# Kernel tuning notes

Measured on AMD Instinct MI355X. Metric: run time of the kernel, lower is better.

The kernel has to match this reference:

```python
import jax, jax.numpy as jnp
import numpy as np

NUM_HEADS = 32
KV_HEADS = 8
HEAD_DIM = 64
HIDDEN = 2048
ROPE_THETA = 10000.0


def setup_inputs() -> dict:
    key = jax.random.key(0)
    ks = jax.random.split(key, 5)
    B, S, H = 2, 2048, HIDDEN
    scale = 0.02
    return {
        "x": jax.random.normal(ks[0], (B, S, H), dtype=jnp.float32),
        # weights stored as (in_features, out_features)
        "Wq": jax.random.normal(ks[1], (H, NUM_HEADS * HEAD_DIM), dtype=jnp.float32) * scale,
        "Wk": jax.random.normal(ks[2], (H, KV_HEADS * HEAD_DIM), dtype=jnp.float32) * scale,
        "Wv": jax.random.normal(ks[3], (H, KV_HEADS * HEAD_DIM), dtype=jnp.float32) * scale,
        "Wo": jax.random.normal(ks[4], (H, H), dtype=jnp.float32) * scale,
    }


def _rope_tables(seq_len, dtype):
    # freq over even dims, angles concatenated twice -> (S, HEAD_DIM)
    freq = 1.0 / (ROPE_THETA ** (jnp.arange(0, HEAD_DIM, 2, dtype=jnp.float32) / HEAD_DIM))
    ang = jnp.arange(seq_len, dtype=jnp.float32)[:, None] * freq[None, :]
    emb = jnp.concatenate([ang, ang], axis=-1)
    return jnp.cos(emb).astype(dtype), jnp.sin(emb).astype(dtype)


def _rotate_half(x):
    x1, x2 = jnp.split(x, 2, axis=-1)
    return jnp.concatenate([-x2, x1], axis=-1)


def reference(x, Wq, Wk, Wv, Wo):
    B, S, H = x.shape
    q = jnp.einsum("bsd,df->bsf", x, Wq).reshape(B, S, NUM_HEADS, HEAD_DIM).transpose(0, 2, 1, 3)
    k = jnp.einsum("bsd,df->bsf", x, Wk).reshape(B, S, KV_HEADS, HEAD_DIM).transpose(0, 2, 1, 3)
    v = jnp.einsum("bsd,df->bsf", x, Wv).reshape(B, S, KV_HEADS, HEAD_DIM).transpose(0, 2, 1, 3)

    cos, sin = _rope_tables(S, x.dtype)  # (S, HEAD_DIM), broadcasts over (B, h, S, D)
    q = q * cos + _rotate_half(q) * sin
    k = k * cos + _rotate_half(k) * sin

    n_rep = NUM_HEADS // KV_HEADS
    k = jnp.repeat(k, n_rep, axis=1)  # (B, NUM_HEADS, S, D)
    v = jnp.repeat(v, n_rep, axis=1)

    scores = jnp.einsum("bhsd,bhtd->bhst", q, k) / jnp.sqrt(jnp.asarray(HEAD_DIM, x.dtype))
    weights = jax.nn.softmax(scores, axis=-1)
    ctx = jnp.einsum("bhst,bhtd->bhsd", weights, v)
    ctx = ctx.transpose(0, 2, 1, 3).reshape(B, S, H)
    return jnp.einsum("bsd,df->bsf", ctx, Wo)
```

## Files before the change

### kernel.cpp

```cpp
#include <hip/hip_runtime.h>

typedef short s8v __attribute__((ext_vector_type(8)));
typedef short s4v __attribute__((ext_vector_type(4)));
typedef unsigned u4v __attribute__((ext_vector_type(4)));
typedef int i2v __attribute__((ext_vector_type(2)));
typedef float f2v __attribute__((ext_vector_type(2)));
typedef float f4v __attribute__((ext_vector_type(4)));

typedef const __attribute__((address_space(1))) char* gp1_t;
typedef __attribute__((address_space(3))) char* lp3_t;

__device__ __forceinline__ float bf2f(short s) {
    union { unsigned u; float f; } c;
    c.u = ((unsigned)(unsigned short)s) << 16;
    return c.f;
}
__device__ __forceinline__ short f2bf(float f) {
    union { float f; unsigned u; } c; c.f = f;
    unsigned r = (c.u + 0x7FFFu + ((c.u >> 16) & 1u)) >> 16;
    return (short)r;
}
__device__ __forceinline__ unsigned cvt_pk_bf16(float a, float b) {
    unsigned r;
    asm("v_cvt_pk_bf16_f32 %0, %1, %2" : "=v"(r) : "v"(a), "v"(b));
    return r;
}
__device__ __forceinline__ s8v cvt8(const float* __restrict__ p) {
    f4v a = *(const f4v*)p;
    f4v b = *(const f4v*)(p + 4);
    s8v r;
    r[0] = f2bf(a[0]); r[1] = f2bf(a[1]); r[2] = f2bf(a[2]); r[3] = f2bf(a[3]);
    r[4] = f2bf(b[0]); r[5] = f2bf(b[1]); r[6] = f2bf(b[2]); r[7] = f2bf(b[3]);
    return r;
}


__global__ __launch_bounds__(256) void cvt_x(const float* __restrict__ x,
                                             short* __restrict__ xb) {
    long i = ((long)blockIdx.x * 256 + threadIdx.x) * 8;
    *(s8v*)&xb[i] = cvt8(&x[i]);
}

__global__ __launch_bounds__(256) void cvt_wt(const float* __restrict__ W,
                                              short* __restrict__ Wt,
                                              int N, int obase, float scale) {
    __shared__ __align__(16) short tile[64 * 72];
    const int kt = blockIdx.y * 64, n0 = blockIdx.x * 64;
    const int t = threadIdx.x;
    const int r = t >> 4, c4 = (t & 15) * 4;
#pragma unroll
    for (int i = 0; i < 4; i++) {
        int kr = r + i * 16;
        f4v v = *(const f4v*)&W[(long)(kt + kr) * N + n0 + c4];
#pragma unroll
        for (int j = 0; j < 4; j++) tile[(c4 + j) * 72 + kr] = f2bf(v[j] * scale);
    }
    __syncthreads();
    const int nr = t >> 3, kc = (t & 7) * 8;
#pragma unroll
    for (int i = 0; i < 2; i++) {
        int n = nr + i * 32;
        *(s8v*)&Wt[(long)(obase + n0 + n) * 2048 + kt + kc] = *(const s8v*)&tile[n * 72 + kc];
    }
}

template <bool CF32, bool ROPE>
__global__ __launch_bounds__(512, 2) void gemm_bt8(const short* __restrict__ A,
                                                   const short* __restrict__ Bt,
                                                   void* __restrict__ Cv,
                                                   int K, int lda, int ldb, int ldc) {
    __shared__ __align__(16) short Ab[2][16384];
    __shared__ __align__(16) short Bb[2][16384];

    const int tid = threadIdx.x;
    const int lane = tid & 63;
    const int wave = tid >> 6;
    const int quad = lane >> 4;
    const int l15 = lane & 15;

    const int nwg = gridDim.x * gridDim.y;
    int f = blockIdx.y * gridDim.x + blockIdx.x;
    if ((nwg & 7) == 0) f = (f & 7) * (nwg >> 3) + (f >> 3);
    const int m0 = (f / gridDim.x) * 256;
    const int n0 = (f % gridDim.x) * 256;

    const int wm = (wave >> 2) * 128;
    const int wn = (wave & 3) * 64;

    const int rsub = lane >> 3;
    const int sslot = (lane & 7) ^ rsub;
    const short* aS[2][2];
    const short* bS[2][2];
#pragma unroll
    for (int h = 0; h < 2; h++)
#pragma unroll
        for (int i = 0; i < 2; i++) {
            int row = h * 128 + wave * 16 + i * 8 + rsub;
            aS[h][i] = A  + (long)(m0 + row) * lda + sslot * 8;
            bS[h][i] = Bt + (long)(n0 + row) * ldb + sslot * 8;
        }

    auto stageA = [&](int buf, int h, int kt) {
        char* d = (char*)&Ab[buf][0] + h * 16384 + wave * 2048;
        __builtin_amdgcn_global_load_lds((gp1_t)(aS[h][0] + (long)kt * 64), (lp3_t)d, 16, 0, 0);
        __builtin_amdgcn_global_load_lds((gp1_t)(aS[h][1] + (long)kt * 64), (lp3_t)(d + 1024), 16, 0, 0);
    };
    auto stageB = [&](int buf, int h, int kt) {
        char* d = (char*)&Bb[buf][0] + h * 16384 + wave * 2048;
        __builtin_amdgcn_global_load_lds((gp1_t)(bS[h][0] + (long)kt * 64), (lp3_t)d, 16, 0, 0);
        __builtin_amdgcn_global_load_lds((gp1_t)(bS[h][1] + (long)kt * 64), (lp3_t)(d + 1024), 16, 0, 0);
    };

    const int ks0 = (quad ^ (l15 & 7)) * 8;
    const int ks1 = ks0 ^ 32;

    f4v acc[2][4][2][2];
#pragma unroll
    for (int a = 0; a < 2; a++)
#pragma unroll
        for (int b = 0; b < 4; b++)
#pragma unroll
            for (int c = 0; c < 2; c++)
#pragma unroll
                for (int d = 0; d < 2; d++) acc[a][b][c][d] = (f4v){0.f, 0.f, 0.f, 0.f};

    const int NT = K >> 6;

    stageB(0, 0, 0); stageB(0, 1, 0); stageA(0, 0, 0); stageA(0, 1, 0);
    stageB(1, 0, 1); stageB(1, 1, 1); stageA(1, 0, 1);
    asm volatile("s_waitcnt vmcnt(6)" ::: "memory");
    __builtin_amdgcn_s_barrier();

    for (int t = 0; t < NT; ++t) {
        const short* Ac = &Ab[t & 1][0];
        const short* Bc = &Bb[t & 1][0];
        const int nb = (t + 1) & 1;
        s8v af[4][2], bf0[2][2], bf1[2][2];

#pragma unroll
        for (int mi = 0; mi < 4; mi++) {
            const int row = wm + mi * 16 + l15;
            af[mi][0] = *(const s8v*)&Ac[row * 64 + ks0];
            af[mi][1] = *(const s8v*)&Ac[row * 64 + ks1];
        }
#pragma unroll
        for (int ni = 0; ni < 2; ni++) {
            const int row = wn + ni * 16 + l15;
            bf0[ni][0] = *(const s8v*)&Bc[row * 64 + ks0];
            bf0[ni][1] = *(const s8v*)&Bc[row * 64 + ks1];
        }
        if (t + 1 < NT) stageA(nb, 1, t + 1);
        __builtin_amdgcn_s_setprio(1);
#pragma unroll
        for (int mi = 0; mi < 4; mi++)
#pragma unroll
            for (int ni = 0; ni < 2; ni++) {
                acc[0][mi][0][ni] = __builtin_amdgcn_mfma_f32_16x16x32_bf16(af[mi][0], bf0[ni][0], acc[0][mi][0][ni], 0, 0, 0);
                acc[0][mi][0][ni] = __builtin_amdgcn_mfma_f32_16x16x32_bf16(af[mi][1], bf0[ni][1], acc[0][mi][0][ni], 0, 0, 0);
            }
        __builtin_amdgcn_s_setprio(0);
        __builtin_amdgcn_s_barrier();

#pragma unroll
        for (int ni = 0; ni < 2; ni++) {
            const int row = wn + 32 + ni * 16 + l15;
            bf1[ni][0] = *(const s8v*)&Bc[row * 64 + ks0];
            bf1[ni][1] = *(const s8v*)&Bc[row * 64 + ks1];
        }
        __builtin_amdgcn_s_setprio(1);
#pragma unroll
        for (int mi = 0; mi < 4; mi++)
#pragma unroll
            for (int ni = 0; ni < 2; ni++) {
                acc[0][mi][1][ni] = __builtin_amdgcn_mfma_f32_16x16x32_bf16(af[mi][0], bf1[ni][0], acc[0][mi][1][ni], 0, 0, 0);
                acc[0][mi][1][ni] = __builtin_amdgcn_mfma_f32_16x16x32_bf16(af[mi][1], bf1[ni][1], acc[0][mi][1][ni], 0, 0, 0);
            }
        __builtin_amdgcn_s_setprio(0);
        __builtin_amdgcn_s_barrier();

#pragma unroll
        for (int mi = 0; mi < 4; mi++) {
            const int row = wm + 64 + mi * 16 + l15;
            af[mi][0] = *(const s8v*)&Ac[row * 64 + ks0];
            af[mi][1] = *(const s8v*)&Ac[row * 64 + ks1];
        }
        if (t + 2 < NT) stageB(t & 1, 0, t + 2);
        __builtin_amdgcn_s_setprio(1);
#pragma unroll
        for (int mi = 0; mi < 4; mi++)
#pragma unroll
            for (int ni = 0; ni < 2; ni++) {
                acc[1][mi][0][ni] = __builtin_amdgcn_mfma_f32_16x16x32_bf16(af[mi][0], bf0[ni][0], acc[1][mi][0][ni], 0, 0, 0);
                acc[1][mi][0][ni] = __builtin_amdgcn_mfma_f32_16x16x32_bf16(af[mi][1], bf0[ni][1], acc[1][mi][0][ni], 0, 0, 0);
            }
        __builtin_amdgcn_s_setprio(0);
        __builtin_amdgcn_s_barrier();

        if (t + 2 < NT) { stageB(t & 1, 1, t + 2); stageA(t & 1, 0, t + 2); }
        __builtin_amdgcn_s_setprio(1);
#pragma unroll
        for (int mi = 0; mi < 4; mi++)
#pragma unroll
            for (int ni = 0; ni < 2; ni++) {
                acc[1][mi][1][ni] = __builtin_amdgcn_mfma_f32_16x16x32_bf16(af[mi][0], bf1[ni][0], acc[1][mi][1][ni], 0, 0, 0);
                acc[1][mi][1][ni] = __builtin_amdgcn_mfma_f32_16x16x32_bf16(af[mi][1], bf1[ni][1], acc[1][mi][1][ni], 0, 0, 0);
            }
        __builtin_amdgcn_s_setprio(0);
        if (t + 1 < NT) {
            if (t + 1 == NT - 1) asm volatile("s_waitcnt vmcnt(0)" ::: "memory");
            else                 asm volatile("s_waitcnt vmcnt(6)" ::: "memory");
            __builtin_amdgcn_s_barrier();
        }
    }

    if (ROPE && (n0 + wn) < 2560) {
        const float NLOG = -0.4152410118609203f;
        const float fr0 = exp2f((float)l15 * NLOG);
        const float fr1 = exp2f((float)(16 + l15) * NLOG);
#pragma unroll
        for (int qm = 0; qm < 2; qm++)
#pragma unroll
            for (int mi = 0; mi < 4; mi++)
#pragma unroll
                for (int r = 0; r < 4; r++) {
                    const float s = (float)((m0 + wm + qm * 64 + mi * 16 + quad * 4 + r) & 2047);
#pragma unroll
                    for (int ni = 0; ni < 2; ni++) {
                        float sn, cs;
                        __sincosf(s * (ni ? fr1 : fr0), &sn, &cs);
                        float x1 = acc[qm][mi][0][ni][r];
                        float x2 = acc[qm][mi][1][ni][r];
                        acc[qm][mi][0][ni][r] = x1 * cs - x2 * sn;
                        acc[qm][mi][1][ni][r] = x2 * cs + x1 * sn;
                    }
                }
    }

#pragma unroll
    for (int qm = 0; qm < 2; qm++)
#pragma unroll
        for (int mi = 0; mi < 4; mi++)
#pragma unroll
            for (int qn = 0; qn < 2; qn++)
#pragma unroll
                for (int ni = 0; ni < 2; ni++)
#pragma unroll
                    for (int r = 0; r < 4; r++) {
                        int row = m0 + wm + qm * 64 + mi * 16 + quad * 4 + r;
                        int col = n0 + wn + qn * 32 + ni * 16 + l15;
                        float v = acc[qm][mi][qn][ni][r];
                        if (CF32) ((float*)Cv)[(long)row * ldc + col] = v;
                        else      ((short*)Cv)[(long)row * ldc + col] = f2bf(v);
                    }
}

template <bool CF32>
__global__ __launch_bounds__(512, 2) void gemm_bt2(const short* __restrict__ A,
                                                   const short* __restrict__ Bt,
                                                   void* __restrict__ Cv,
                                                   int K, int lda, int ldb, int ldc) {
    __shared__ __align__(16) short Ab[2][8192];
    __shared__ __align__(16) short Bb[2][16384];

    const int tid = threadIdx.x;
    const int lane = tid & 63;
    const int wave = tid >> 6;
    const int quad = lane >> 4;
    const int l15 = lane & 15;

    const int nwg = gridDim.x * gridDim.y;
    int f = blockIdx.y * gridDim.x + blockIdx.x;
    if ((nwg & 7) == 0) f = (f & 7) * (nwg >> 3) + (f >> 3);
    const int m0 = (f / gridDim.x) * 128;
    const int n0 = (f % gridDim.x) * 256;

    const int wm = (wave >> 2) * 64;
    const int wn = (wave & 3) * 64;

    const int rsub = lane >> 3;
    const int sslot = (lane & 7) ^ rsub;
    const short* aS[2];
    const short* bS[4];
#pragma unroll
    for (int i = 0; i < 2; i++)
        aS[i] = A + (long)(m0 + wave * 16 + i * 8 + rsub) * lda + sslot * 8;
#pragma unroll
    for (int i = 0; i < 4; i++)
        bS[i] = Bt + (long)(n0 + wave * 32 + i * 8 + rsub) * ldb + sslot * 8;

    auto stageA = [&](int buf, int kt) {
        char* d = (char*)&Ab[buf][0] + wave * 2048;
        __builtin_amdgcn_global_load_lds((gp1_t)(aS[0] + (long)kt * 64), (lp3_t)d, 16, 0, 0);
        __builtin_amdgcn_global_load_lds((gp1_t)(aS[1] + (long)kt * 64), (lp3_t)(d + 1024), 16, 0, 0);
    };
    auto stageBh = [&](int buf, int h, int kt) {
        char* d = (char*)&Bb[buf][0] + wave * 4096 + h * 2048;
        __builtin_amdgcn_global_load_lds((gp1_t)(bS[2 * h] + (long)kt * 64), (lp3_t)d, 16, 0, 0);
        __builtin_amdgcn_global_load_lds((gp1_t)(bS[2 * h + 1] + (long)kt * 64), (lp3_t)(d + 1024), 16, 0, 0);
    };

    const int ks0 = (quad ^ (l15 & 7)) * 8;
    const int ks1 = ks0 ^ 32;

    f4v acc[4][2][2];
#pragma unroll
    for (int a = 0; a < 4; a++)
#pragma unroll
        for (int b = 0; b < 2; b++)
#pragma unroll
            for (int c = 0; c < 2; c++) acc[a][b][c] = (f4v){0.f, 0.f, 0.f, 0.f};

    const int NT = K >> 6;

    stageA(0, 0); stageBh(0, 0, 0); stageBh(0, 1, 0);
    stageA(1, 1); stageBh(1, 0, 1); stageBh(1, 1, 1);
    asm volatile("s_waitcnt vmcnt(6)" ::: "memory");
    __builtin_amdgcn_s_barrier();

    for (int t = 0; t < NT; ++t) {
        const short* Ac = &Ab[t & 1][0];
        const short* Bc = &Bb[t & 1][0];
        s8v af01[2][2], af23[2][2], bf0[2][2], bf1[2][2];

#pragma unroll
        for (int mi = 0; mi < 2; mi++) {
            const int row = wm + mi * 16 + l15;
            af01[mi][0] = *(const s8v*)&Ac[row * 64 + ks0];
            af01[mi][1] = *(const s8v*)&Ac[row * 64 + ks1];
        }
#pragma unroll
        for (int ni = 0; ni < 2; ni++) {
            const int row = wn + ni * 16 + l15;
            bf0[ni][0] = *(const s8v*)&Bc[row * 64 + ks0];
            bf0[ni][1] = *(const s8v*)&Bc[row * 64 + ks1];
        }
        __builtin_amdgcn_s_setprio(1);
#pragma unroll
        for (int mi = 0; mi < 2; mi++)
#pragma unroll
            for (int ni = 0; ni < 2; ni++) {
                acc[mi][0][ni] = __builtin_amdgcn_mfma_f32_16x16x32_bf16(af01[mi][0], bf0[ni][0], acc[mi][0][ni], 0, 0, 0);
                acc[mi][0][ni] = __builtin_amdgcn_mfma_f32_16x16x32_bf16(af01[mi][1], bf0[ni][1], acc[mi][0][ni], 0, 0, 0);
            }
        __builtin_amdgcn_s_setprio(0);
        __builtin_amdgcn_s_barrier();

#pragma unroll
        for (int ni = 0; ni < 2; ni++) {
            const int row = wn + 32 + ni * 16 + l15;
            bf1[ni][0] = *(const s8v*)&Bc[row * 64 + ks0];
            bf1[ni][1] = *(const s8v*)&Bc[row * 64 + ks1];
        }
        if (t + 2 < NT) stageBh(t & 1, 0, t + 2);
        __builtin_amdgcn_s_setprio(1);
#pragma unroll
        for (int mi = 0; mi < 2; mi++)
#pragma unroll
            for (int ni = 0; ni < 2; ni++) {
                acc[mi][1][ni] = __builtin_amdgcn_mfma_f32_16x16x32_bf16(af01[mi][0], bf1[ni][0], acc[mi][1][ni], 0, 0, 0);
                acc[mi][1][ni] = __builtin_amdgcn_mfma_f32_16x16x32_bf16(af01[mi][1], bf1[ni][1], acc[mi][1][ni], 0, 0, 0);
            }
        __builtin_amdgcn_s_setprio(0);
        __builtin_amdgcn_s_barrier();

#pragma unroll
        for (int mi = 0; mi < 2; mi++) {
            const int row = wm + 32 + mi * 16 + l15;
            af23[mi][0] = *(const s8v*)&Ac[row * 64 + ks0];
            af23[mi][1] = *(const s8v*)&Ac[row * 64 + ks1];
        }
        if (t + 2 < NT) stageBh(t & 1, 1, t + 2);
        __builtin_amdgcn_s_setprio(1);
#pragma unroll
        for (int mi = 0; mi < 2; mi++)
#pragma unroll
            for (int ni = 0; ni < 2; ni++) {
                acc[2 + mi][0][ni] = __builtin_amdgcn_mfma_f32_16x16x32_bf16(af23[mi][0], bf0[ni][0], acc[2 + mi][0][ni], 0, 0, 0);
                acc[2 + mi][0][ni] = __builtin_amdgcn_mfma_f32_16x16x32_bf16(af23[mi][1], bf0[ni][1], acc[2 + mi][0][ni], 0, 0, 0);
            }
        __builtin_amdgcn_s_setprio(0);
        __builtin_amdgcn_s_barrier();

        if (t + 2 < NT) stageA(t & 1, t + 2);
        __builtin_amdgcn_s_setprio(1);
#pragma unroll
        for (int mi = 0; mi < 2; mi++)
#pragma unroll
            for (int ni = 0; ni < 2; ni++) {
                acc[2 + mi][1][ni] = __builtin_amdgcn_mfma_f32_16x16x32_bf16(af23[mi][0], bf1[ni][0], acc[2 + mi][1][ni], 0, 0, 0);
                acc[2 + mi][1][ni] = __builtin_amdgcn_mfma_f32_16x16x32_bf16(af23[mi][1], bf1[ni][1], acc[2 + mi][1][ni], 0, 0, 0);
            }
        __builtin_amdgcn_s_setprio(0);
        if (t + 1 < NT) {
            if (t + 1 == NT - 1) asm volatile("s_waitcnt vmcnt(0)" ::: "memory");
            else                 asm volatile("s_waitcnt vmcnt(6)" ::: "memory");
            __builtin_amdgcn_s_barrier();
        }
    }

#pragma unroll
    for (int mi = 0; mi < 4; mi++)
#pragma unroll
        for (int qn = 0; qn < 2; qn++)
#pragma unroll
            for (int ni = 0; ni < 2; ni++)
#pragma unroll
                for (int r = 0; r < 4; r++) {
                    int row = m0 + wm + mi * 16 + quad * 4 + r;
                    int col = n0 + wn + qn * 32 + ni * 16 + l15;
                    float v = acc[mi][qn][ni][r];
                    if (CF32) ((float*)Cv)[(long)row * ldc + col] = v;
                    else      ((short*)Cv)[(long)row * ldc + col] = f2bf(v);
                }
}

__global__ __launch_bounds__(256) void rope_kernel(short* __restrict__ qkv) {
    int tid = blockIdx.x * 256 + threadIdx.x;
    int p = tid % 1280;
    int row = tid / 1280;
    int head = p >> 5;
    int j = p & 31;
    int s = row & 2047;
    int c1 = head * 64 + j;
    float freq = exp2f(-(float)j * 0.4152410118609203f);
    float ang = (float)s * freq;
    float sn, cs;
    __sincosf(ang, &sn, &cs);
    long base = (long)row * 3072;
    float x1 = bf2f(qkv[base + c1]);
    float x2 = bf2f(qkv[base + c1 + 32]);
    qkv[base + c1]      = f2bf(x1 * cs - x2 * sn);
    qkv[base + c1 + 32] = f2bf(x2 * cs + x1 * sn);
}

__global__ __launch_bounds__(256) void vtrans(const short* __restrict__ qkv,
                                              short* __restrict__ Vt_g) {
    __shared__ __align__(16) short tile[64 * 72];
    const int kt = blockIdx.x * 64;
    const int kvh = blockIdx.y;
    const int b = blockIdx.z;
    const int t = threadIdx.x;
#pragma unroll
    for (int cc = 0; cc < 2; cc++) {
        int ch = t + cc * 256;
        int key = ch >> 3, d0 = (ch & 7) * 8;
        s8v v = *(const s8v*)&qkv[(long)(b * 2048 + kt + key) * 3072 + 2560 + kvh * 64 + d0];
#pragma unroll
        for (int i = 0; i < 8; i++) tile[(d0 + i) * 72 + key] = v[i];
    }
    __syncthreads();
#pragma unroll
    for (int cc = 0; cc < 2; cc++) {
        int ch = t + cc * 256;
        int d = ch >> 3, c = ch & 7;
        int base1 = 32 * (c >> 2) + 4 * (c & 3);
        s4v lo = *(const s4v*)&tile[d * 72 + base1];
        s4v hi = *(const s4v*)&tile[d * 72 + base1 + 16];
        s8v w;
        w[0] = lo[0]; w[1] = lo[1]; w[2] = lo[2]; w[3] = lo[3];
        w[4] = hi[0]; w[5] = hi[1]; w[6] = hi[2]; w[7] = hi[3];
        *(s8v*)&Vt_g[(long)((b * 8 + kvh) * 64 + d) * 2048 + kt + c * 8] = w;
    }
}

__global__ __launch_bounds__(256, 4) void attn5(short* __restrict__ qkv,
                                                const short* __restrict__ Vt_g) {
    __shared__ __align__(16) short KV[2][2][4096];
    __shared__ float rsb[4][32];

    const int tid = threadIdx.x;
    const int lane = tid & 63;
    const int wave = tid >> 6;
    const int quad = lane >> 4;
    const int l15 = lane & 15;

    int f = (blockIdx.z * 32 + blockIdx.y) * 16 + blockIdx.x;
    f = (f & 7) * 128 + (f >> 3);
    const int b = f >> 9;
    const int h = (f >> 4) & 31;
    const int kvh = h >> 2;
    const int q0 = (f & 15) * 128;

    const long kbase = ((long)b * 2048) * 3072 + 2048 + kvh * 64;
    const long vtbase = (long)(b * 8 + kvh) * 64 * 2048;

    const long qrow = (long)b * 2048 + q0 + wave * 32 + l15;
    const short* qp = qkv + qrow * 3072 + h * 64 + quad * 8;
    const s8v qf00 = *(const s8v*)(qp);
    const s8v qf01 = *(const s8v*)(qp + 32);
    const s8v qf10 = *(const s8v*)(qp + 16 * 3072);
    const s8v qf11 = *(const s8v*)(qp + 16 * 3072 + 32);

    const int rA = wave * 8 + (lane >> 3);
    const int sslot = (lane & 7) ^ (lane >> 3);
    const short* kA = qkv + kbase + (long)rA * 3072 + sslot * 8;
    const short* kB = kA + (long)32 * 3072;
    const short* vA = Vt_g + vtbase + (long)rA * 2048 + sslot * 8;
    const short* vB = vA + (long)32 * 2048;

    {
        char* kd = (char*)&KV[0][0][0] + wave * 1024;
        char* vd = (char*)&KV[0][1][0] + wave * 1024;
        __builtin_amdgcn_global_load_lds((gp1_t)kA, (lp3_t)kd, 16, 0, 0);
        __builtin_amdgcn_global_load_lds((gp1_t)kB, (lp3_t)(kd + 4096), 16, 0, 0);
        __builtin_amdgcn_global_load_lds((gp1_t)vA, (lp3_t)vd, 16, 0, 0);
        __builtin_amdgcn_global_load_lds((gp1_t)vB, (lp3_t)(vd + 4096), 16, 0, 0);
    }
    __syncthreads();

    const int ks0 = ((quad ^ (l15 & 7)) << 3);
    const int ks1 = ks0 ^ 32;

    f2v rs0v = (f2v){0.f, 0.f}, rs1v = (f2v){0.f, 0.f};
    f4v o0[4], o1[4];
#pragma unroll
    for (int ni = 0; ni < 4; ni++) { o0[ni] = (f4v){0.f, 0.f, 0.f, 0.f}; o1[ni] = (f4v){0.f, 0.f, 0.f, 0.f}; }

    for (int t = 0; t < 32; ++t) {
        const short* Kb = &KV[t & 1][0][0];
        const short* Vb = &KV[t & 1][1][0];

        if (t < 31) {
            const long ko = (long)(t + 1) * (64 * 3072);
            const long vo = (long)(t + 1) * 64;
            char* kd = (char*)&KV[(t + 1) & 1][0][0] + wave * 1024;
            char* vd = (char*)&KV[(t + 1) & 1][1][0] + wave * 1024;
            __builtin_amdgcn_global_load_lds((gp1_t)(kA + ko), (lp3_t)kd, 16, 0, 0);
            __builtin_amdgcn_global_load_lds((gp1_t)(kB + ko), (lp3_t)(kd + 4096), 16, 0, 0);
            __builtin_amdgcn_global_load_lds((gp1_t)(vA + vo), (lp3_t)vd, 16, 0, 0);
            __builtin_amdgcn_global_load_lds((gp1_t)(vB + vo), (lp3_t)(vd + 4096), 16, 0, 0);
        }

        unsigned pk0[4][2], pk1[4][2];
#pragma unroll
        for (int ni = 0; ni < 4; ni++) {
            const int ro = (ni * 16 + l15) * 64;
            const s8v kf0 = *(const s8v*)&Kb[ro + ks0];
            const s8v kf1 = *(const s8v*)&Kb[ro + ks1];
            f4v a = (f4v){-24.f, -24.f, -24.f, -24.f};
            a = __builtin_amdgcn_mfma_f32_16x16x32_bf16(kf0, qf00, a, 0, 0, 0);
            a = __builtin_amdgcn_mfma_f32_16x16x32_bf16(kf1, qf01, a, 0, 0, 0);
            {
                float p0 = exp2f(a[0]);
                float p1 = exp2f(a[1]);
                float p2 = exp2f(a[2]);
                float p3 = exp2f(a[3]);
                rs0v += (f2v){p0, p1};
                rs0v += (f2v){p2, p3};
                pk0[ni][0] = cvt_pk_bf16(p0, p1);
                pk0[ni][1] = cvt_pk_bf16(p2, p3);
            }
            f4v c = (f4v){-24.f, -24.f, -24.f, -24.f};
            c = __builtin_amdgcn_mfma_f32_16x16x32_bf16(kf0, qf10, c, 0, 0, 0);
            c = __builtin_amdgcn_mfma_f32_16x16x32_bf16(kf1, qf11, c, 0, 0, 0);
            {
                float p0 = exp2f(c[0]);
                float p1 = exp2f(c[1]);
                float p2 = exp2f(c[2]);
                float p3 = exp2f(c[3]);
                rs1v += (f2v){p0, p1};
                rs1v += (f2v){p2, p3};
                pk1[ni][0] = cvt_pk_bf16(p0, p1);
                pk1[ni][1] = cvt_pk_bf16(p2, p3);
            }
        }

        union PU { u4v u; s8v s; };
        PU pa0, pa1, pb0, pb1;
        pa0.u = (u4v){pk0[0][0], pk0[0][1], pk0[1][0], pk0[1][1]};
        pa1.u = (u4v){pk0[2][0], pk0[2][1], pk0[3][0], pk0[3][1]};
        pb0.u = (u4v){pk1[0][0], pk1[0][1], pk1[1][0], pk1[1][1]};
        pb1.u = (u4v){pk1[2][0], pk1[2][1], pk1[3][0], pk1[3][1]};

#pragma unroll
        for (int ni = 0; ni < 4; ni++) {
            const int ro = (ni * 16 + l15) * 64;
            const s8v vf0 = *(const s8v*)&Vb[ro + ks0];
            const s8v vf1 = *(const s8v*)&Vb[ro + ks1];
            o0[ni] = __builtin_amdgcn_mfma_f32_16x16x32_bf16(pa0.s, vf0, o0[ni], 0, 0, 0);
            o0[ni] = __builtin_amdgcn_mfma_f32_16x16x32_bf16(pa1.s, vf1, o0[ni], 0, 0, 0);
            o1[ni] = __builtin_amdgcn_mfma_f32_16x16x32_bf16(pb0.s, vf0, o1[ni], 0, 0, 0);
            o1[ni] = __builtin_amdgcn_mfma_f32_16x16x32_bf16(pb1.s, vf1, o1[ni], 0, 0, 0);
        }
        __syncthreads();
    }

    float rs0 = rs0v[0] + rs0v[1];
    float rs1 = rs1v[0] + rs1v[1];
    rs0 += __shfl_xor(rs0, 16); rs0 += __shfl_xor(rs0, 32);
    rs1 += __shfl_xor(rs1, 16); rs1 += __shfl_xor(rs1, 32);
    if (quad == 0) { rsb[wave][l15] = rs0; rsb[wave][16 + l15] = rs1; }
    __syncthreads();

#pragma unroll
    for (int r = 0; r < 4; r++) {
        const float i0 = 1.0f / rsb[wave][quad * 4 + r];
        const float i1 = 1.0f / rsb[wave][16 + quad * 4 + r];
        const long ob0 = ((long)b * 2048 + q0 + wave * 32 + quad * 4 + r) * 3072 + h * 64;
        const long ob1 = ob0 + 16 * 3072;
#pragma unroll
        for (int ni = 0; ni < 4; ni++) {
            qkv[ob0 + ni * 16 + l15] = f2bf(o0[ni][r] * i0);
            qkv[ob1 + ni * 16 + l15] = f2bf(o1[ni][r] * i1);
        }
    }
}


template <bool AF32, bool CF32>
__global__ __launch_bounds__(256) void gemm_bn(const void* __restrict__ Av,
                                               const float* __restrict__ B,
                                               void* __restrict__ Cv,
                                               int K, int N, int lda, int ldc) {
    __shared__ __align__(16) short As[128 * 40];
    __shared__ __align__(16) short Bs[128 * 40];
    const int tid = threadIdx.x;
    const int lane = tid & 63;
    const int wave = tid >> 6;
    const int quad = lane >> 4;
    const int l15 = lane & 15;
    const int m0 = blockIdx.y * 128;
    const int n0 = blockIdx.x * 128;
    const int wm = (wave & 1) * 64;
    const int wn = (wave >> 1) * 64;

    f4v acc[4][4];
#pragma unroll
    for (int i = 0; i < 4; i++)
#pragma unroll
        for (int j = 0; j < 4; j++) acc[i][j] = (f4v){0.f, 0.f, 0.f, 0.f};

    const int ar0 = tid >> 2, akc0 = (tid & 3) * 8;
    const int ar1 = (tid + 256) >> 2, akc1 = ((tid + 256) & 3) * 8;
    const int bk0 = tid >> 4, bnc0 = (tid & 15) * 8;
    const int bk1 = (tid + 256) >> 4, bnc1 = ((tid + 256) & 15) * 8;

    for (int k0 = 0; k0 < K; k0 += 32) {
        __syncthreads();
        if (AF32) {
            const float* A = (const float*)Av;
            *(s8v*)(&As[ar0 * 40 + akc0]) = cvt8(&A[(long)(m0 + ar0) * lda + k0 + akc0]);
            *(s8v*)(&As[ar1 * 40 + akc1]) = cvt8(&A[(long)(m0 + ar1) * lda + k0 + akc1]);
        } else {
            const short* A = (const short*)Av;
            *(s8v*)(&As[ar0 * 40 + akc0]) = *(const s8v*)(&A[(long)(m0 + ar0) * lda + k0 + akc0]);
            *(s8v*)(&As[ar1 * 40 + akc1]) = *(const s8v*)(&A[(long)(m0 + ar1) * lda + k0 + akc1]);
        }
        s8v b0 = cvt8(&B[(long)(k0 + bk0) * N + n0 + bnc0]);
        s8v b1 = cvt8(&B[(long)(k0 + bk1) * N + n0 + bnc1]);
#pragma unroll
        for (int i = 0; i < 8; i++) Bs[(bnc0 + i) * 40 + bk0] = b0[i];
#pragma unroll
        for (int i = 0; i < 8; i++) Bs[(bnc1 + i) * 40 + bk1] = b1[i];
        __syncthreads();
        s8v af[4], bfr[4];
#pragma unroll
        for (int mi = 0; mi < 4; mi++)
            af[mi] = *(const s8v*)(&As[(wm + mi * 16 + l15) * 40 + quad * 8]);
#pragma unroll
        for (int ni = 0; ni < 4; ni++)
            bfr[ni] = *(const s8v*)(&Bs[(wn + ni * 16 + l15) * 40 + quad * 8]);
#pragma unroll
        for (int mi = 0; mi < 4; mi++)
#pragma unroll
            for (int ni = 0; ni < 4; ni++)
                acc[mi][ni] = __builtin_amdgcn_mfma_f32_16x16x32_bf16(af[mi], bfr[ni], acc[mi][ni], 0, 0, 0);
    }
#pragma unroll
    for (int mi = 0; mi < 4; mi++)
#pragma unroll
        for (int ni = 0; ni < 4; ni++)
#pragma unroll
            for (int r = 0; r < 4; r++) {
                int row = m0 + wm + mi * 16 + quad * 4 + r;
                int col = n0 + wn + ni * 16 + l15;
                if (CF32) ((float*)Cv)[(long)row * ldc + col] = acc[mi][ni][r];
                else      ((short*)Cv)[(long)row * ldc + col] = f2bf(acc[mi][ni][r]);
            }
}

__global__ __launch_bounds__(256) void attn_kernel(short* __restrict__ qkv) {
    __shared__ __align__(16) short Qs[64 * 72];
    __shared__ __align__(16) short Ks[64 * 72];
    __shared__ __align__(16) short Vt[64 * 72];
    __shared__ __align__(16) short Ps[4][16 * 72];

    const int tid = threadIdx.x;
    const int lane = tid & 63;
    const int wave = tid >> 6;
    const int quad = lane >> 4;
    const int l15 = lane & 15;
    const int b = blockIdx.z;
    const int h = blockIdx.y;
    const int kvh = h >> 2;
    const int q0 = blockIdx.x * 64;

    const long qbase = ((long)b * 2048 + q0) * 3072 + h * 64;
    const long kbase = ((long)b * 2048) * 3072 + 2048 + kvh * 64;
    const long vbase = kbase + 512;

#pragma unroll
    for (int cc = 0; cc < 2; cc++) {
        int ch = tid + cc * 256;
        int r = ch >> 3, d0 = (ch & 7) * 8;
        *(s8v*)(&Qs[r * 72 + d0]) = *(const s8v*)(&qkv[qbase + (long)r * 3072 + d0]);
    }
    __syncthreads();
    s8v qf[2];
    qf[0] = *(const s8v*)(&Qs[(wave * 16 + l15) * 72 + quad * 8]);
    qf[1] = *(const s8v*)(&Qs[(wave * 16 + l15) * 72 + 32 + quad * 8]);

    float m_i[4], l_i[4];
    f4v o[4];
#pragma unroll
    for (int r = 0; r < 4; r++) { m_i[r] = -1e30f; l_i[r] = 0.0f; }
#pragma unroll
    for (int ni = 0; ni < 4; ni++) o[ni] = (f4v){0.f, 0.f, 0.f, 0.f};

    for (int kt = 0; kt < 2048; kt += 64) {
        __syncthreads();
#pragma unroll
        for (int cc = 0; cc < 2; cc++) {
            int ch = tid + cc * 256;
            int r = ch >> 3, d0 = (ch & 7) * 8;
            *(s8v*)(&Ks[r * 72 + d0]) = *(const s8v*)(&qkv[kbase + (long)(kt + r) * 3072 + d0]);
            s8v v = *(const s8v*)(&qkv[vbase + (long)(kt + r) * 3072 + d0]);
            int g = d0 >> 3;
            int chn = ((r >> 3) ^ g) * 8 + (r & 7);
#pragma unroll
            for (int i = 0; i < 8; i++) Vt[(d0 + i) * 72 + chn] = v[i];
        }
        __syncthreads();

        f4v sc[4];
#pragma unroll
        for (int ni = 0; ni < 4; ni++) {
            s8v kf0 = *(const s8v*)(&Ks[(ni * 16 + l15) * 72 + quad * 8]);
            s8v kf1 = *(const s8v*)(&Ks[(ni * 16 + l15) * 72 + 32 + quad * 8]);
            f4v a = (f4v){0.f, 0.f, 0.f, 0.f};
            a = __builtin_amdgcn_mfma_f32_16x16x32_bf16(qf[0], kf0, a, 0, 0, 0);
            a = __builtin_amdgcn_mfma_f32_16x16x32_bf16(qf[1], kf1, a, 0, 0, 0);
            sc[ni] = a * 0.125f;
        }
        float alpha[4], rs[4];
#pragma unroll
        for (int r = 0; r < 4; r++) {
            float v = fmaxf(fmaxf(sc[0][r], sc[1][r]), fmaxf(sc[2][r], sc[3][r]));
            v = fmaxf(v, __shfl_xor(v, 1));
            v = fmaxf(v, __shfl_xor(v, 2));
            v = fmaxf(v, __shfl_xor(v, 4));
            v = fmaxf(v, __shfl_xor(v, 8));
            float mn = fmaxf(m_i[r], v);
            alpha[r] = __expf(m_i[r] - mn);
            m_i[r] = mn;
            rs[r] = 0.f;
        }
#pragma unroll
        for (int ni = 0; ni < 4; ni++)
#pragma unroll
            for (int r = 0; r < 4; r++) {
                float pv = __expf(sc[ni][r] - m_i[r]);
                sc[ni][r] = pv;
                rs[r] += pv;
            }
#pragma unroll
        for (int r = 0; r < 4; r++) {
            float v = rs[r];
            v += __shfl_xor(v, 1);
            v += __shfl_xor(v, 2);
            v += __shfl_xor(v, 4);
            v += __shfl_xor(v, 8);
            l_i[r] = l_i[r] * alpha[r] + v;
        }
#pragma unroll
        for (int ni = 0; ni < 4; ni++)
#pragma unroll
            for (int r = 0; r < 4; r++) {
                int row = quad * 4 + r;
                int key = ni * 16 + l15;
                int chn = ((key >> 3) ^ (row >> 3)) * 8 + (key & 7);
                Ps[wave][row * 72 + chn] = f2bf(sc[ni][r]);
            }
        __syncthreads();
#pragma unroll
        for (int ni = 0; ni < 4; ni++) {
            f4v t = o[ni];
            t[0] *= alpha[0]; t[1] *= alpha[1]; t[2] *= alpha[2]; t[3] *= alpha[3];
            o[ni] = t;
        }
        s8v pf0 = *(const s8v*)(&Ps[wave][l15 * 72 + ((quad ^ (l15 >> 3)) * 8)]);
        s8v pf1 = *(const s8v*)(&Ps[wave][l15 * 72 + (((4 + quad) ^ (l15 >> 3)) * 8)]);
#pragma unroll
        for (int ni = 0; ni < 4; ni++) {
            int d = ni * 16 + l15;
            s8v vf0 = *(const s8v*)(&Vt[d * 72 + ((quad ^ (d >> 3)) * 8)]);
            s8v vf1 = *(const s8v*)(&Vt[d * 72 + (((4 + quad) ^ (d >> 3)) * 8)]);
            o[ni] = __builtin_amdgcn_mfma_f32_16x16x32_bf16(pf0, vf0, o[ni], 0, 0, 0);
            o[ni] = __builtin_amdgcn_mfma_f32_16x16x32_bf16(pf1, vf1, o[ni], 0, 0, 0);
        }
    }
#pragma unroll
    for (int r = 0; r < 4; r++) {
        float inv = 1.0f / l_i[r];
        int srow = q0 + wave * 16 + quad * 4 + r;
        long obase = ((long)b * 2048 + srow) * 3072 + h * 64;
#pragma unroll
        for (int ni = 0; ni < 4; ni++)
            qkv[obase + ni * 16 + l15] = f2bf(o[ni][r] * inv);
    }
}

extern "C" void kernel_launch(void* const* d_in, const int* in_sizes, int n_in,
                              void* d_out, int out_size, void* d_ws, size_t ws_size,
                              hipStream_t stream) {
    (void)in_sizes; (void)n_in; (void)out_size;
    const float* x  = (const float*)d_in[0];
    const float* Wq = (const float*)d_in[1];
    const float* Wk = (const float*)d_in[2];
    const float* Wv = (const float*)d_in[3];
    const float* Wo = (const float*)d_in[4];

    const float CS = 0.18033688011112042f;
    const size_t need = 67108864ULL;
    if (ws_size >= need) {
        short* xb    = (short*)d_ws;
        short* Wqkvt = xb + 8388608;
        short* Wot   = Wqkvt + 6291456;
        short* qkv   = Wot + 4194304;
        short* Vt_g  = qkv + 12582912;

        cvt_x<<<4096, 256, 0, stream>>>(x, xb);
        cvt_wt<<<dim3(32, 32), 256, 0, stream>>>(Wq, Wqkvt, 2048, 0, 1.0f);
        cvt_wt<<<dim3(8, 32), 256, 0, stream>>>(Wk, Wqkvt, 512, 2048, CS);
        cvt_wt<<<dim3(8, 32), 256, 0, stream>>>(Wv, Wqkvt, 512, 2560, 1.0f);
        cvt_wt<<<dim3(32, 32), 256, 0, stream>>>(Wo, Wot, 2048, 0, 1.0f);
        gemm_bt8<false, true><<<dim3(12, 16), 512, 0, stream>>>(xb, Wqkvt, qkv, 2048, 2048, 2048, 3072);
        vtrans<<<dim3(32, 8, 2), 256, 0, stream>>>(qkv, Vt_g);
        attn5<<<dim3(16, 32, 2), 256, 0, stream>>>(qkv, Vt_g);
        gemm_bt2<true><<<dim3(8, 32), 512, 0, stream>>>(qkv, Wot, d_out, 2048, 3072, 2048, 2048);
    } else {
        short* qkv = (short*)d_ws;
        gemm_bn<true, false><<<dim3(16, 32), 256, 0, stream>>>(x, Wq, qkv,        2048, 2048, 2048, 3072);
        gemm_bn<true, false><<<dim3(4, 32), 256, 0, stream>>>(x, Wk, qkv + 2048, 2048,  512, 2048, 3072);
        gemm_bn<true, false><<<dim3(4, 32), 256, 0, stream>>>(x, Wv, qkv + 2560, 2048,  512, 2048, 3072);
        rope_kernel<<<dim3(20480), 256, 0, stream>>>(qkv);
        attn_kernel<<<dim3(32, 32, 2), 256, 0, stream>>>(qkv);
        gemm_bn<false, true><<<dim3(16, 32), 256, 0, stream>>>(qkv, Wo, d_out, 2048, 2048, 3072, 2048);
    }
}
```

Baseline: 314.8 us.

## Merge conversion kernels and compute softmax row sums with MFMA

Merges the five input and weight bf16 conversion launches into one prep kernel that dispatches on block index. In the attention kernel, the probability row sums are now computed by extra MFMAs against a vector of bf16 ones, not by scalar adds followed by shuffles and an LDS reduction. The launch-bounds occupancy hint goes from 4 to 5 blocks. The intent is to cut launch overhead and VALU work, at the cost of four more MFMAs per tile and row sums taken from bf16-rounded probabilities.

```diff
diff --git a/kernel.cpp b/kernel.cpp
--- a/kernel.cpp
+++ b/kernel.cpp
@@ -3,8 +3,6 @@
 typedef short s8v __attribute__((ext_vector_type(8)));
 typedef short s4v __attribute__((ext_vector_type(4)));
 typedef unsigned u4v __attribute__((ext_vector_type(4)));
-typedef int i2v __attribute__((ext_vector_type(2)));
-typedef float f2v __attribute__((ext_vector_type(2)));
 typedef float f4v __attribute__((ext_vector_type(4)));
 
 typedef const __attribute__((address_space(1))) char* gp1_t;
@@ -35,17 +33,27 @@
 }
 
 
-__global__ __launch_bounds__(256) void cvt_x(const float* __restrict__ x,
-                                             short* __restrict__ xb) {
-    long i = ((long)blockIdx.x * 256 + threadIdx.x) * 8;
-    *(s8v*)&xb[i] = cvt8(&x[i]);
-}
-
-__global__ __launch_bounds__(256) void cvt_wt(const float* __restrict__ W,
-                                              short* __restrict__ Wt,
-                                              int N, int obase, float scale) {
+__global__ __launch_bounds__(256) void prep(const float* __restrict__ x,
+                                            const float* __restrict__ Wq,
+                                            const float* __restrict__ Wk,
+                                            const float* __restrict__ Wv,
+                                            const float* __restrict__ Wo,
+                                            short* __restrict__ xb,
+                                            short* __restrict__ Wqkvt,
+                                            short* __restrict__ Wot) {
     __shared__ __align__(16) short tile[64 * 72];
-    const int kt = blockIdx.y * 64, n0 = blockIdx.x * 64;
+    int id = blockIdx.x;
+    if (id >= 2560) {
+        long i = ((long)(id - 2560) * 256 + threadIdx.x) * 8;
+        *(s8v*)&xb[i] = cvt8(&x[i]);
+        return;
+    }
+    const float* W; short* Wt; int N, obase, nx; float scale;
+    if (id < 1024)      { W = Wq; Wt = Wqkvt; N = 2048; obase = 0;    nx = 32; scale = 1.0f; }
+    else if (id < 1280) { W = Wk; Wt = Wqkvt; N = 512;  obase = 2048; nx = 8;  scale = 0.18033688011112042f; id -= 1024; }
+    else if (id < 1536) { W = Wv; Wt = Wqkvt; N = 512;  obase = 2560; nx = 8;  scale = 1.0f; id -= 1280; }
+    else                { W = Wo; Wt = Wot;   N = 2048; obase = 0;    nx = 32; scale = 1.0f; id -= 1536; }
+    const int kt = (id / nx) * 64, n0 = (id % nx) * 64;
     const int t = threadIdx.x;
     const int r = t >> 4, c4 = (t & 15) * 4;
 #pragma unroll
@@ -463,10 +471,9 @@
     }
 }
 
-__global__ __launch_bounds__(256, 4) void attn5(short* __restrict__ qkv,
+__global__ __launch_bounds__(256, 5) void attn6(short* __restrict__ qkv,
                                                 const short* __restrict__ Vt_g) {
     __shared__ __align__(16) short KV[2][2][4096];
-    __shared__ float rsb[4][32];
 
     const int tid = threadIdx.x;
     const int lane = tid & 63;
@@ -511,8 +518,11 @@
     const int ks0 = ((quad ^ (l15 & 7)) << 3);
     const int ks1 = ks0 ^ 32;
 
-    f2v rs0v = (f2v){0.f, 0.f}, rs1v = (f2v){0.f, 0.f};
+    const s8v vones = (s8v){16256, 16256, 16256, 16256, 16256, 16256, 16256, 16256};
+
     f4v o0[4], o1[4];
+    f4v ors0 = (f4v){0.f, 0.f, 0.f, 0.f};
+    f4v ors1 = (f4v){0.f, 0.f, 0.f, 0.f};
 #pragma unroll
     for (int ni = 0; ni < 4; ni++) { o0[ni] = (f4v){0.f, 0.f, 0.f, 0.f}; o1[ni] = (f4v){0.f, 0.f, 0.f, 0.f}; }
 
@@ -541,27 +551,15 @@
             a = __builtin_amdgcn_mfma_f32_16x16x32_bf16(kf0, qf00, a, 0, 0, 0);
             a = __builtin_amdgcn_mfma_f32_16x16x32_bf16(kf1, qf01, a, 0, 0, 0);
             {
-                float p0 = exp2f(a[0]);
-                float p1 = exp2f(a[1]);
-                float p2 = exp2f(a[2]);
-                float p3 = exp2f(a[3]);
-                rs0v += (f2v){p0, p1};
-                rs0v += (f2v){p2, p3};
-                pk0[ni][0] = cvt_pk_bf16(p0, p1);
-                pk0[ni][1] = cvt_pk_bf16(p2, p3);
+                pk0[ni][0] = cvt_pk_bf16(exp2f(a[0]), exp2f(a[1]));
+                pk0[ni][1] = cvt_pk_bf16(exp2f(a[2]), exp2f(a[3]));
             }
             f4v c = (f4v){-24.f, -24.f, -24.f, -24.f};
             c = __builtin_amdgcn_mfma_f32_16x16x32_bf16(kf0, qf10, c, 0, 0, 0);
             c = __builtin_amdgcn_mfma_f32_16x16x32_bf16(kf1, qf11, c, 0, 0, 0);
             {
-                float p0 = exp2f(c[0]);
-                float p1 = exp2f(c[1]);
-                float p2 = exp2f(c[2]);
-                float p3 = exp2f(c[3]);
-                rs1v += (f2v){p0, p1};
-                rs1v += (f2v){p2, p3};
-                pk1[ni][0] = cvt_pk_bf16(p0, p1);
-                pk1[ni][1] = cvt_pk_bf16(p2, p3);
+                pk1[ni][0] = cvt_pk_bf16(exp2f(c[0]), exp2f(c[1]));
+                pk1[ni][1] = cvt_pk_bf16(exp2f(c[2]), exp2f(c[3]));
             }
         }
 
@@ -571,6 +569,11 @@
         pa1.u = (u4v){pk0[2][0], pk0[2][1], pk0[3][0], pk0[3][1]};
         pb0.u = (u4v){pk1[0][0], pk1[0][1], pk1[1][0], pk1[1][1]};
         pb1.u = (u4v){pk1[2][0], pk1[2][1], pk1[3][0], pk1[3][1]};
+
+        ors0 = __builtin_amdgcn_mfma_f32_16x16x32_bf16(pa0.s, vones, ors0, 0, 0, 0);
+        ors0 = __builtin_amdgcn_mfma_f32_16x16x32_bf16(pa1.s, vones, ors0, 0, 0, 0);
+        ors1 = __builtin_amdgcn_mfma_f32_16x16x32_bf16(pb0.s, vones, ors1, 0, 0, 0);
+        ors1 = __builtin_amdgcn_mfma_f32_16x16x32_bf16(pb1.s, vones, ors1, 0, 0, 0);
 
 #pragma unroll
         for (int ni = 0; ni < 4; ni++) {
@@ -585,17 +588,10 @@
         __syncthreads();
     }
 
-    float rs0 = rs0v[0] + rs0v[1];
-    float rs1 = rs1v[0] + rs1v[1];
-    rs0 += __shfl_xor(rs0, 16); rs0 += __shfl_xor(rs0, 32);
-    rs1 += __shfl_xor(rs1, 16); rs1 += __shfl_xor(rs1, 32);
-    if (quad == 0) { rsb[wave][l15] = rs0; rsb[wave][16 + l15] = rs1; }
-    __syncthreads();
-
 #pragma unroll
     for (int r = 0; r < 4; r++) {
-        const float i0 = 1.0f / rsb[wave][quad * 4 + r];
-        const float i1 = 1.0f / rsb[wave][16 + quad * 4 + r];
+        const float i0 = 1.0f / ors0[r];
+        const float i1 = 1.0f / ors1[r];
         const long ob0 = ((long)b * 2048 + q0 + wave * 32 + quad * 4 + r) * 3072 + h * 64;
         const long ob1 = ob0 + 16 * 3072;
 #pragma unroll
@@ -820,7 +816,6 @@
     const float* Wv = (const float*)d_in[3];
     const float* Wo = (const float*)d_in[4];
 
-    const float CS = 0.18033688011112042f;
     const size_t need = 67108864ULL;
     if (ws_size >= need) {
         short* xb    = (short*)d_ws;
@@ -829,14 +824,10 @@
         short* qkv   = Wot + 4194304;
         short* Vt_g  = qkv + 12582912;
 
-        cvt_x<<<4096, 256, 0, stream>>>(x, xb);
-        cvt_wt<<<dim3(32, 32), 256, 0, stream>>>(Wq, Wqkvt, 2048, 0, 1.0f);
-        cvt_wt<<<dim3(8, 32), 256, 0, stream>>>(Wk, Wqkvt, 512, 2048, CS);
-        cvt_wt<<<dim3(8, 32), 256, 0, stream>>>(Wv, Wqkvt, 512, 2560, 1.0f);
-        cvt_wt<<<dim3(32, 32), 256, 0, stream>>>(Wo, Wot, 2048, 0, 1.0f);
+        prep<<<6656, 256, 0, stream>>>(x, Wq, Wk, Wv, Wo, xb, Wqkvt, Wot);
         gemm_bt8<false, true><<<dim3(12, 16), 512, 0, stream>>>(xb, Wqkvt, qkv, 2048, 2048, 2048, 3072);
         vtrans<<<dim3(32, 8, 2), 256, 0, stream>>>(qkv, Vt_g);
-        attn5<<<dim3(16, 32, 2), 256, 0, stream>>>(qkv, Vt_g);
+        attn6<<<dim3(16, 32, 2), 256, 0, stream>>>(qkv, Vt_g);
         gemm_bt2<true><<<dim3(8, 32), 512, 0, stream>>>(qkv, Wot, d_out, 2048, 3072, 2048, 2048);
     } else {
         short* qkv = (short*)d_ws;
```

Measured after the change: 333.3 us. 1.06x slower.
